# Kernel tuning notes

Measured on AMD Instinct MI355X. Metric: run time of the kernel, lower is better.

## Reference

```python
import jax, jax.numpy as jnp
import numpy as np

B, C, CI, H, W = 4, 256, 128, 64, 64  # batch, in_channels, inter_channels, spatial
EPS = 1e-5


def conv1x1(x, w, b):
    # x: [b,c,h,w], w: [o,c], b: [o] -> [b,o,h,w]
    return jnp.einsum('bchw,oc->bohw', x, w) + b[None, :, None, None]


def setup_inputs() -> dict:
    key = jax.random.key(0)
    ks = jax.random.split(key, 16)
    s_in = 1.0 / np.sqrt(C)
    s_mid = 1.0 / np.sqrt(CI)
    inp = {
        'feats_all': jax.random.normal(ks[0], (B, C, H, W), dtype=jnp.float32),
        'human_feats': jax.random.normal(ks[1], (B, C, H, W), dtype=jnp.float32),
        'g_w': jax.random.uniform(ks[2], (CI, C), jnp.float32, -s_in, s_in),
        'g_b': jax.random.uniform(ks[3], (CI,), jnp.float32, -s_in, s_in),
        'theta_w': jax.random.uniform(ks[4], (CI, C), jnp.float32, -s_in, s_in),
        'theta_b': jax.random.uniform(ks[5], (CI,), jnp.float32, -s_in, s_in),
        'phi_w': jax.random.uniform(ks[6], (CI, C), jnp.float32, -s_in, s_in),
        'phi_b': jax.random.uniform(ks[7], (CI,), jnp.float32, -s_in, s_in),
        'human_theta_w': jax.random.uniform(ks[8], (CI, C), jnp.float32, -s_in, s_in),
        'human_theta_b': jax.random.uniform(ks[9], (CI,), jnp.float32, -s_in, s_in),
        'human_phi_w': jax.random.uniform(ks[10], (CI, C), jnp.float32, -s_in, s_in),
        'human_phi_b': jax.random.uniform(ks[11], (CI,), jnp.float32, -s_in, s_in),
        'W_w': jax.random.uniform(ks[12], (C, CI), jnp.float32, -s_mid, s_mid),
        'W_b': jax.random.uniform(ks[13], (C,), jnp.float32, -s_mid, s_mid),
        'bn_gamma': jax.random.normal(ks[14], (C,), dtype=jnp.float32) * 0.1 + 1.0,
        'bn_beta': jax.random.normal(ks[15], (C,), dtype=jnp.float32) * 0.1,
        'bn_mean': jnp.zeros((C,), jnp.float32),
        'bn_var': jnp.ones((C,), jnp.float32),
    }
    return inp


def reference(feats_all, human_feats, g_w, g_b, theta_w, theta_b, phi_w, phi_b,
              human_theta_w, human_theta_b, human_phi_w, human_phi_b,
              W_w, W_b, bn_gamma, bn_beta, bn_mean, bn_var):
    b = feats_all.shape[0]
    n = H * W
    scale = CI ** -0.5

    # human attention map: softmax over keys of scaled QK^T
    hq = conv1x1(human_feats, human_theta_w, human_theta_b).reshape(b, CI, n)  # [b,ci,n]
    hk = conv1x1(human_feats, human_phi_w, human_phi_b).reshape(b, CI, n)
    human_map = jax.nn.softmax(scale * jnp.einsum('bcq,bck->bqk', hq, hk), axis=-1)

    # standard non-local map on feats_all
    th = conv1x1(feats_all, theta_w, theta_b).reshape(b, CI, n)
    ph = conv1x1(feats_all, phi_w, phi_b).reshape(b, CI, n)
    f = jax.nn.softmax(scale * jnp.einsum('bcq,bck->bqk', th, ph), axis=-1)

    g_x = conv1x1(feats_all, g_w, g_b).reshape(b, CI, n)  # [b,ci,n]

    attn = (human_map + f) * 0.5                          # [b,n,n]
    y = jnp.einsum('bqk,bck->bcq', attn, g_x)             # [b,ci,n]
    y = y.reshape(b, CI, H, W)

    wy = conv1x1(y, W_w, W_b)                             # [b,C,H,W]
    # BatchNorm2d (eval mode, running stats)
    inv = bn_gamma / jnp.sqrt(bn_var + EPS)
    out = (wy - bn_mean[None, :, None, None]) * inv[None, :, None, None] + bn_beta[None, :, None, None]
    return out
```

## Files before the change

### kernel.cpp

```cpp
#include <hip/hip_runtime.h>

#define DEVI __device__ __forceinline__

typedef float f32x4 __attribute__((ext_vector_type(4)));
typedef unsigned int u32x4 __attribute__((ext_vector_type(4)));
typedef unsigned int u32x2 __attribute__((ext_vector_type(2)));
typedef __bf16 bf16x8 __attribute__((ext_vector_type(8)));

#define NB 4
#define CIN 256
#define CI_ 128
#define NN 4096
#define SCALE 0.08838834764831845f

typedef unsigned short us;

DEVI us f2bf(float f) {
  unsigned int x = __float_as_uint(f);
  x += 0x7FFFu + ((x >> 16) & 1u);
  return (us)(x >> 16);
}

DEVI unsigned pack2(float a, float b) {
  return (unsigned)f2bf(a) | ((unsigned)f2bf(b) << 16);
}

DEVI f32x4 mfma16(u32x4 a, u32x4 b, f32x4 c) {
  return __builtin_amdgcn_mfma_f32_16x16x32_bf16(
      __builtin_bit_cast(bf16x8, a), __builtin_bit_cast(bf16x8, b), c, 0, 0, 0);
}

DEVI void gload16(const void* g, void* l) {
  __builtin_amdgcn_global_load_lds(
      (const __attribute__((address_space(1))) void*)g,
      (__attribute__((address_space(3))) void*)l, 16, 0, 0);
}

__global__ __launch_bounds__(256) void wcvt_kernel(
    const float* __restrict__ hth_w, const float* __restrict__ hph_w,
    const float* __restrict__ th_w, const float* __restrict__ ph_w,
    const float* __restrict__ g_w, const float* __restrict__ Ww,
    us* __restrict__ wb) {
  const float* srcs[6] = {hth_w, hph_w, th_w, ph_w, g_w, Ww};
  const float* s = srcs[blockIdx.y];
  us* d = wb + blockIdx.y * 32768;
  int idx = (blockIdx.x * 256 + threadIdx.x) * 4;
  f32x4 v = *(const f32x4*)(s + idx);
  u32x2 o;
  o[0] = pack2(v[0], v[1]);
  o[1] = pack2(v[2], v[3]);
  *(u32x2*)(d + idx) = o;
}

__global__ __launch_bounds__(256) void proj_kernel(
    const float* __restrict__ feats, const float* __restrict__ human,
    const float* __restrict__ g_b, const float* __restrict__ th_b,
    const float* __restrict__ ph_b, const float* __restrict__ hth_b,
    const float* __restrict__ hph_b, const us* __restrict__ wb,
    us* __restrict__ hqT, us* __restrict__ hkT,
    us* __restrict__ thT, us* __restrict__ phT, us* __restrict__ gP) {
  __shared__ alignas(16) us xf[64 * 256];
  __shared__ alignas(16) us xh[64 * 256];
  const int t = threadIdx.x;
  const int b = blockIdx.y;
  const int n0 = blockIdx.x * 64;
  const int w = t >> 6, l = t & 63, g16 = l >> 4, l15 = l & 15;

  for (int which = 0; which < 2; ++which) {
    const float* src = which ? human : feats;
    us* dst = which ? xh : xf;
    for (int i = 0; i < 16; ++i) {
      int e = (i * 256 + t) * 4;
      int c = e >> 6, nn = e & 63;
      f32x4 v = *(const f32x4*)(src + (size_t)(b * CIN + c) * NN + n0 + nn);
#pragma unroll
      for (int j = 0; j < 4; ++j) {
        int row = nn + j;
        dst[row * 256 + (c ^ ((row & 15) << 3))] = f2bf(v[j]);
      }
    }
  }
  __syncthreads();

  const float* pb[4] = {hth_b, hph_b, th_b, ph_b};
  us* pout[4] = {hqT, hkT, thT, phT};

  u32x4 afrag[8];
  const int arow = w * 16 + l15;
  for (int p = 0; p < 4; ++p) {
    const us* tile = (p < 2) ? xh : xf;
    if (p == 0 || p == 2) {
#pragma unroll
      for (int s = 0; s < 8; ++s)
        afrag[s] = *(const u32x4*)((const char*)tile + arow * 512 +
                                   (((s << 6) | (g16 << 4)) ^ (l15 << 4)));
    }
    const us* wbp = wb + p * 32768;
    for (int nt = 0; nt < 8; ++nt) {
      f32x4 acc = {0.f, 0.f, 0.f, 0.f};
#pragma unroll
      for (int s = 0; s < 8; ++s) {
        u32x4 bf = *(const u32x4*)(wbp + (nt * 16 + l15) * 256 + s * 32 + g16 * 8);
        acc = mfma16(afrag[s], bf, acc);
      }
      float bias = pb[p][nt * 16 + l15];
#pragma unroll
      for (int r = 0; r < 4; ++r) {
        int nrow = n0 + w * 16 + g16 * 4 + r;
        pout[p][((size_t)b * NN + nrow) * CI_ + nt * 16 + l15] = f2bf(acc[r] + bias);
      }
    }
  }

  const us* wbg = wb + 4 * 32768;
  u32x4 ag[2][8];
#pragma unroll
  for (int mt = 0; mt < 2; ++mt)
#pragma unroll
    for (int s = 0; s < 8; ++s)
      ag[mt][s] = *(const u32x4*)(wbg + (w * 32 + mt * 16 + l15) * 256 + s * 32 + g16 * 8);
  float gb[2][4];
#pragma unroll
  for (int mt = 0; mt < 2; ++mt)
#pragma unroll
    for (int r = 0; r < 4; ++r) gb[mt][r] = g_b[w * 32 + mt * 16 + g16 * 4 + r];
  for (int nt = 0; nt < 4; ++nt) {
    f32x4 acc0 = {0.f, 0.f, 0.f, 0.f}, acc1 = {0.f, 0.f, 0.f, 0.f};
#pragma unroll
    for (int s = 0; s < 8; ++s) {
      u32x4 bf = *(const u32x4*)((const char*)xf + (nt * 16 + l15) * 512 +
                                 ((s * 64 + g16 * 16) ^ (l15 << 4)));
      acc0 = mfma16(ag[0][s], bf, acc0);
      acc1 = mfma16(ag[1][s], bf, acc1);
    }
#pragma unroll
    for (int r = 0; r < 4; ++r) {
      int ci0 = w * 32 + g16 * 4 + r;
      gP[((size_t)b * CI_ + ci0) * NN + n0 + nt * 16 + l15] = f2bf(acc0[r] + gb[0][r]);
      gP[((size_t)b * CI_ + ci0 + 16) * NN + n0 + nt * 16 + l15] = f2bf(acc1[r] + gb[1][r]);
    }
  }
}

__global__ __launch_bounds__(128, 2) void attn_kernel(
    const us* __restrict__ hqT, const us* __restrict__ hkT,
    const us* __restrict__ thT, const us* __restrict__ phT,
    const us* __restrict__ gP, us* __restrict__ PY, float* __restrict__ PL) {
  __shared__ alignas(16) us sK[2][32 * 128];
  __shared__ alignas(16) us sV[2][64 * 64];
  __shared__ alignas(16) us sPp[2][16 * 64];
  const int t = threadIdx.x, w = t >> 6, l = t & 63, g16 = l >> 4, l15 = l & 15;
  const int id = blockIdx.x;
  const int xcd = id & 7, b = xcd & 3, path = xcd >> 2;
  const int r2 = id >> 3, h = r2 & 1, chunk = r2 >> 1;
  const int q0 = chunk * 64, kb = h * 2048;
  const us* Qsrc = path ? thT : hqT;
  const char* Kb = (const char*)(path ? phT : hkT) + (size_t)b * NN * 256;
  const char* Vb = (const char*)gP + (size_t)b * CI_ * NN * 2;

  u32x4 aQ[2][4];
#pragma unroll
  for (int qs = 0; qs < 2; ++qs)
#pragma unroll
    for (int s = 0; s < 4; ++s)
      aQ[qs][s] = *(const u32x4*)(Qsrc +
          ((size_t)b * NN + q0 + w * 32 + qs * 16 + l15) * CI_ + s * 32 + g16 * 8);

  f32x4 Y[2][8];
#pragma unroll
  for (int qs = 0; qs < 2; ++qs)
#pragma unroll
    for (int dt = 0; dt < 8; ++dt) Y[qs][dt] = {0.f, 0.f, 0.f, 0.f};
  float lsum[2] = {0.f, 0.f};

  auto stage = [&](int k0, int buf) {
#pragma unroll
    for (int i = 0; i < 4; ++i) {
      int krow = w * 16 + i * 4 + (l >> 4);
      gload16(Kb + (size_t)(k0 + krow) * 256 + (((l & 15) * 16) ^ ((krow & 7) << 4)),
              (char*)sK[buf] + (w * 16 + i * 4) * 256);
    }
#pragma unroll
    for (int i = 0; i < 4; ++i) {
      int j = w * 32 + i * 8 + (l >> 3);
      int srcin = ((l & 7) * 16) ^ ((j & 7) << 4);
      gload16(Vb + (size_t)(2 * j + (srcin >> 6)) * (NN * 2) + (size_t)k0 * 2 + (srcin & 63),
              (char*)sV[buf] + (w * 32 + i * 8) * 128);
    }
  };

  stage(kb, 0);
  __syncthreads();
  for (int kt = 0; kt < 64; ++kt) {
    const int cur = kt & 1;
    if (kt < 63) stage(kb + (kt + 1) * 32, cur ^ 1);
    const char* sKc = (const char*)sK[cur];
    const char* sVc = (const char*)sV[cur];
    float pv[2][2][4];
#pragma unroll
    for (int nt = 0; nt < 2; ++nt) {
      f32x4 a0 = {0.f, 0.f, 0.f, 0.f}, a1 = {0.f, 0.f, 0.f, 0.f};
#pragma unroll
      for (int s = 0; s < 4; ++s) {
        u32x4 bk = *(const u32x4*)(sKc + (nt * 16 + l15) * 256 +
                                   ((s * 64 + g16 * 16) ^ ((l15 & 7) << 4)));
        a0 = mfma16(bk, aQ[0][s], a0);
        a1 = mfma16(bk, aQ[1][s], a1);
      }
#pragma unroll
      for (int r = 0; r < 4; ++r) {
        float p0 = __expf(a0[r] * SCALE), p1 = __expf(a1[r] * SCALE);
        lsum[0] += p0;
        lsum[1] += p1;
        pv[0][nt][r] = p0;
        pv[1][nt][r] = p1;
      }
    }
#pragma unroll
    for (int qs = 0; qs < 2; ++qs)
#pragma unroll
      for (int nt = 0; nt < 2; ++nt) {
        u32x2 pw;
        pw[0] = pack2(pv[qs][nt][0], pv[qs][nt][1]);
        pw[1] = pack2(pv[qs][nt][2], pv[qs][nt][3]);
        *(u32x2*)((char*)sPp[w] + (qs * 8 + (l15 >> 1)) * 128 +
                  (((l15 & 1) * 64 + nt * 32 + g16 * 8) ^ ((l15 >> 1) << 4))) = pw;
      }
    u32x4 aP[2];
#pragma unroll
    for (int qs = 0; qs < 2; ++qs)
      aP[qs] = *(const u32x4*)((char*)sPp[w] + (qs * 8 + (l15 >> 1)) * 128 +
                               (((l15 & 1) * 64 + g16 * 16) ^ ((l15 >> 1) << 4)));
#pragma unroll
    for (int dt = 0; dt < 8; ++dt) {
      int dd = dt * 16 + l15;
      u32x4 bv = *(const u32x4*)(sVc + (dd >> 1) * 128 +
                                 (((dd & 1) * 64 + g16 * 16) ^ (((dd >> 1) & 7) << 4)));
      Y[0][dt] = mfma16(aP[0], bv, Y[0][dt]);
      Y[1][dt] = mfma16(aP[1], bv, Y[1][dt]);
    }
    __syncthreads();
  }

  const int bp = b * 2 + path;
#pragma unroll
  for (int qs = 0; qs < 2; ++qs) {
    float v = lsum[qs];
    v += __shfl_xor(v, 16);
    v += __shfl_xor(v, 32);
    if (g16 == 0)
      PL[(size_t)(h * 8 + bp) * NN + q0 + w * 32 + qs * 16 + l15] = v;
#pragma unroll
    for (int dt = 0; dt < 8; ++dt)
#pragma unroll
      for (int r = 0; r < 4; ++r)
        PY[(size_t)(h * 8 + bp) * (NN * CI_) +
           (size_t)(q0 + w * 32 + qs * 16 + g16 * 4 + r) * CI_ + dt * 16 + l15] =
            f2bf(Y[qs][dt][r]);
  }
}

__global__ __launch_bounds__(256) void wout_kernel(
    const us* __restrict__ PY, const float* __restrict__ PL,
    const us* __restrict__ wb, const float* __restrict__ Wb,
    const float* __restrict__ gamma, const float* __restrict__ beta,
    const float* __restrict__ mean, const float* __restrict__ var,
    float* __restrict__ out) {
  __shared__ alignas(16) us sY[64 * 128];
  const int t = threadIdx.x, w = t >> 6, l = t & 63, g16 = l >> 4, l15 = l & 15;
  const int n0 = blockIdx.x * 64;
  const int ob = blockIdx.y * 64;
  const int b = blockIdx.z;

  {
    const int row = t >> 2, cg = t & 3;
    const int n = n0 + row;
    float ls[2];
#pragma unroll
    for (int p = 0; p < 2; ++p) {
      int bpi = b * 2 + p;
      ls[p] = 0.5f / (PL[(size_t)bpi * NN + n] + PL[(size_t)(8 + bpi) * NN + n]);
    }
    float acc[32];
#pragma unroll
    for (int e = 0; e < 32; ++e) acc[e] = 0.f;
#pragma unroll
    for (int p = 0; p < 2; ++p) {
      float sc = ls[p];
#pragma unroll
      for (int hh = 0; hh < 2; ++hh) {
        const us* src = PY + (size_t)(hh * 8 + b * 2 + p) * (NN * CI_) +
                        (size_t)n * CI_ + cg * 32;
#pragma unroll
        for (int j = 0; j < 4; ++j) {
          u32x4 v = *(const u32x4*)(src + j * 8);
#pragma unroll
          for (int e = 0; e < 4; ++e) {
            unsigned u = v[e];
            acc[j * 8 + 2 * e] += __uint_as_float(u << 16) * sc;
            acc[j * 8 + 2 * e + 1] += __uint_as_float(u & 0xFFFF0000u) * sc;
          }
        }
      }
    }
#pragma unroll
    for (int j = 0; j < 4; ++j) {
      u32x4 o;
#pragma unroll
      for (int e = 0; e < 4; ++e)
        o[e] = pack2(acc[j * 8 + 2 * e], acc[j * 8 + 2 * e + 1]);
      *(u32x4*)((char*)sY + row * 256 + ((cg * 64 + j * 16) ^ ((row & 7) << 4))) = o;
    }
  }

  const us* wbw = wb + 5 * 32768;
  u32x4 aW[4];
  const int orow = ob + w * 16 + l15;
#pragma unroll
  for (int s = 0; s < 4; ++s)
    aW[s] = *(const u32x4*)(wbw + orow * 128 + s * 32 + g16 * 8);
  float wbias[4], inv_[4], mu[4], bt[4];
#pragma unroll
  for (int r = 0; r < 4; ++r) {
    int o = ob + w * 16 + g16 * 4 + r;
    wbias[r] = Wb[o];
    inv_[r] = gamma[o] * rsqrtf(var[o] + 1e-5f);
    mu[r] = mean[o];
    bt[r] = beta[o];
  }
  __syncthreads();

  for (int nt = 0; nt < 4; ++nt) {
    f32x4 acc = {0.f, 0.f, 0.f, 0.f};
#pragma unroll
    for (int s = 0; s < 4; ++s) {
      u32x4 bf = *(const u32x4*)((const char*)sY + (nt * 16 + l15) * 256 +
                                 (((s << 6) | (g16 << 4)) ^ ((l15 & 7) << 4)));
      acc = mfma16(aW[s], bf, acc);
    }
#pragma unroll
    for (int r = 0; r < 4; ++r) {
      int o = ob + w * 16 + g16 * 4 + r;
      out[((size_t)b * CIN + o) * NN + n0 + nt * 16 + l15] =
          (acc[r] + wbias[r] - mu[r]) * inv_[r] + bt[r];
    }
  }
}

extern "C" void kernel_launch(void* const* d_in, const int* in_sizes, int n_in,
                              void* d_out, int out_size, void* d_ws, size_t ws_size,
                              hipStream_t stream) {
  const float* feats = (const float*)d_in[0];
  const float* human = (const float*)d_in[1];
  const float* g_w = (const float*)d_in[2];
  const float* g_b = (const float*)d_in[3];
  const float* th_w = (const float*)d_in[4];
  const float* th_b = (const float*)d_in[5];
  const float* ph_w = (const float*)d_in[6];
  const float* ph_b = (const float*)d_in[7];
  const float* hth_w = (const float*)d_in[8];
  const float* hth_b = (const float*)d_in[9];
  const float* hph_w = (const float*)d_in[10];
  const float* hph_b = (const float*)d_in[11];
  const float* Ww = (const float*)d_in[12];
  const float* Wb = (const float*)d_in[13];
  const float* gamma = (const float*)d_in[14];
  const float* beta = (const float*)d_in[15];
  const float* mean = (const float*)d_in[16];
  const float* var = (const float*)d_in[17];

  us* ws = (us*)d_ws;
  const size_t SZ = (size_t)NB * NN * CI_;
  us* hqT = ws;
  us* hkT = ws + SZ;
  us* thT = ws + 2 * SZ;
  us* phT = ws + 3 * SZ;
  us* gP = ws + 4 * SZ;
  us* PY = ws + 5 * SZ;
  float* PL = (float*)(ws + 5 * SZ + 8388608);
  us* wb = ws + 5 * SZ + 8388608 + 131072;

  wcvt_kernel<<<dim3(32, 6), 256, 0, stream>>>(hth_w, hph_w, th_w, ph_w, g_w, Ww, wb);
  proj_kernel<<<dim3(64, 4), 256, 0, stream>>>(feats, human, g_b, th_b, ph_b,
                                               hth_b, hph_b, wb, hqT, hkT, thT,
                                               phT, gP);
  attn_kernel<<<1024, 128, 0, stream>>>(hqT, hkT, thT, phT, gP, PY, PL);
  wout_kernel<<<dim3(64, 4, 4), 256, 0, stream>>>(PY, PL, wb, Wb, gamma, beta,
                                                  mean, var, (float*)d_out);
}
```

Before: 157.2 us.

## Restructure attention kernel with larger key tiles, in-block key split, exp2 prescale

The attention kernel now uses 256-thread blocks that each own 64 queries across all keys. The four waves split each 128-key tile, and their partial outputs are reduced through shared memory instead of being written as two half-range partials to global memory. The softmax scale times log2(e) is folded into the Q projection so the kernel can call a raw exp2. Float-to-bf16 packing uses the hardware v_cvt_pk_bf16_f32 instruction, and the projection input staging loads two channels per thread to pack pairs. This cuts global partial traffic and raises MFMA reuse per loaded K/V tile, at the cost of more registers, a single-buffered stage with extra barriers, and a shared-memory reduction epilogue.

```diff
diff --git a/kernel.cpp b/kernel.cpp
--- a/kernel.cpp
+++ b/kernel.cpp
@@ -11,7 +11,7 @@
 #define CIN 256
 #define CI_ 128
 #define NN 4096
-#define SCALE 0.08838834764831845f
+#define QSCALE 0.12752792233895158f
 
 typedef unsigned short us;
 
@@ -21,8 +21,18 @@
   return (us)(x >> 16);
 }
 
-DEVI unsigned pack2(float a, float b) {
-  return (unsigned)f2bf(a) | ((unsigned)f2bf(b) << 16);
+DEVI unsigned cvtpk(float lo, float hi) {
+  unsigned r;
+  asm("v_cvt_pk_bf16_f32 %0, %1, %2" : "=v"(r) : "v"(lo), "v"(hi));
+  return r;
+}
+
+DEVI float exp2fast(float x) {
+#if __has_builtin(__builtin_amdgcn_exp2f)
+  return __builtin_amdgcn_exp2f(x);
+#else
+  return exp2f(x);
+#endif
 }
 
 DEVI f32x4 mfma16(u32x4 a, u32x4 b, f32x4 c) {
@@ -47,8 +57,8 @@
   int idx = (blockIdx.x * 256 + threadIdx.x) * 4;
   f32x4 v = *(const f32x4*)(s + idx);
   u32x2 o;
-  o[0] = pack2(v[0], v[1]);
-  o[1] = pack2(v[2], v[3]);
+  o[0] = cvtpk(v[0], v[1]);
+  o[1] = cvtpk(v[2], v[3]);
   *(u32x2*)(d + idx) = o;
 }
 
@@ -65,18 +75,22 @@
   const int b = blockIdx.y;
   const int n0 = blockIdx.x * 64;
   const int w = t >> 6, l = t & 63, g16 = l >> 4, l15 = l & 15;
+  const int tg = t >> 4, tl = t & 15;
 
   for (int which = 0; which < 2; ++which) {
     const float* src = which ? human : feats;
     us* dst = which ? xh : xf;
-    for (int i = 0; i < 16; ++i) {
-      int e = (i * 256 + t) * 4;
-      int c = e >> 6, nn = e & 63;
-      f32x4 v = *(const f32x4*)(src + (size_t)(b * CIN + c) * NN + n0 + nn);
+#pragma unroll
+    for (int i = 0; i < 8; ++i) {
+      int p = i * 16 + tg;
+      const float* s0 = src + (size_t)(b * CIN + 2 * p) * NN + n0 + tl * 4;
+      f32x4 v0 = *(const f32x4*)s0;
+      f32x4 v1 = *(const f32x4*)(s0 + NN);
 #pragma unroll
       for (int j = 0; j < 4; ++j) {
-        int row = nn + j;
-        dst[row * 256 + (c ^ ((row & 15) << 3))] = f2bf(v[j]);
+        int row = tl * 4 + j;
+        *(unsigned*)((char*)dst + row * 512 + ((4 * p) ^ ((row & 15) << 4))) =
+            cvtpk(v0[j], v1[j]);
       }
     }
   }
@@ -96,6 +110,7 @@
                                    (((s << 6) | (g16 << 4)) ^ (l15 << 4)));
     }
     const us* wbp = wb + p * 32768;
+    const float scl = (p == 0 || p == 2) ? QSCALE : 1.0f;
     for (int nt = 0; nt < 8; ++nt) {
       f32x4 acc = {0.f, 0.f, 0.f, 0.f};
 #pragma unroll
@@ -107,7 +122,8 @@
 #pragma unroll
       for (int r = 0; r < 4; ++r) {
         int nrow = n0 + w * 16 + g16 * 4 + r;
-        pout[p][((size_t)b * NN + nrow) * CI_ + nt * 16 + l15] = f2bf(acc[r] + bias);
+        pout[p][((size_t)b * NN + nrow) * CI_ + nt * 16 + l15] =
+            f2bf((acc[r] + bias) * scl);
       }
     }
   }
@@ -142,121 +158,185 @@
   }
 }
 
-__global__ __launch_bounds__(128, 2) void attn_kernel(
+__global__ __launch_bounds__(256, 2) void attn_kernel(
     const us* __restrict__ hqT, const us* __restrict__ hkT,
     const us* __restrict__ thT, const us* __restrict__ phT,
     const us* __restrict__ gP, us* __restrict__ PY, float* __restrict__ PL) {
-  __shared__ alignas(16) us sK[2][32 * 128];
-  __shared__ alignas(16) us sV[2][64 * 64];
-  __shared__ alignas(16) us sPp[2][16 * 64];
+  __shared__ alignas(16) us sK[128 * 128];
+  __shared__ alignas(16) us sV[128 * 128];
+  __shared__ alignas(16) us sP[64 * 128];
+
   const int t = threadIdx.x, w = t >> 6, l = t & 63, g16 = l >> 4, l15 = l & 15;
   const int id = blockIdx.x;
-  const int xcd = id & 7, b = xcd & 3, path = xcd >> 2;
-  const int r2 = id >> 3, h = r2 & 1, chunk = r2 >> 1;
-  const int q0 = chunk * 64, kb = h * 2048;
-  const us* Qsrc = path ? thT : hqT;
-  const char* Kb = (const char*)(path ? phT : hkT) + (size_t)b * NN * 256;
-  const char* Vb = (const char*)gP + (size_t)b * CI_ * NN * 2;
-
-  u32x4 aQ[2][4];
-#pragma unroll
-  for (int qs = 0; qs < 2; ++qs)
+  const int bp = id & 7, b = bp & 3, path = bp >> 2;
+  const int q0 = (id >> 3) * 64;
+  const us* Qs = (path ? thT : hqT) + (size_t)b * NN * CI_;
+  const char* Kb = (const char*)((path ? phT : hkT) + (size_t)b * NN * CI_);
+  const char* Vb = (const char*)(gP + (size_t)b * CI_ * NN);
+
+  u32x4 aQ[4][4];
+#pragma unroll
+  for (int qs = 0; qs < 4; ++qs)
 #pragma unroll
     for (int s = 0; s < 4; ++s)
-      aQ[qs][s] = *(const u32x4*)(Qsrc +
-          ((size_t)b * NN + q0 + w * 32 + qs * 16 + l15) * CI_ + s * 32 + g16 * 8);
-
-  f32x4 Y[2][8];
-#pragma unroll
-  for (int qs = 0; qs < 2; ++qs)
+      aQ[qs][s] = *(const u32x4*)(Qs + (size_t)(q0 + qs * 16 + l15) * CI_ +
+                                  s * 32 + g16 * 8);
+
+  f32x4 Y[4][8];
+#pragma unroll
+  for (int qs = 0; qs < 4; ++qs)
 #pragma unroll
     for (int dt = 0; dt < 8; ++dt) Y[qs][dt] = {0.f, 0.f, 0.f, 0.f};
-  float lsum[2] = {0.f, 0.f};
-
-  auto stage = [&](int k0, int buf) {
-#pragma unroll
-    for (int i = 0; i < 4; ++i) {
-      int krow = w * 16 + i * 4 + (l >> 4);
-      gload16(Kb + (size_t)(k0 + krow) * 256 + (((l & 15) * 16) ^ ((krow & 7) << 4)),
-              (char*)sK[buf] + (w * 16 + i * 4) * 256);
-    }
-#pragma unroll
-    for (int i = 0; i < 4; ++i) {
-      int j = w * 32 + i * 8 + (l >> 3);
-      int srcin = ((l & 7) * 16) ^ ((j & 7) << 4);
-      gload16(Vb + (size_t)(2 * j + (srcin >> 6)) * (NN * 2) + (size_t)k0 * 2 + (srcin & 63),
-              (char*)sV[buf] + (w * 32 + i * 8) * 128);
+  float lsum[4] = {0.f, 0.f, 0.f, 0.f};
+
+  const int rr = w * 32 + (l >> 4);
+  const int uK = l & 15;
+
+  auto stage = [&](int k0) {
+#pragma unroll
+    for (int i = 0; i < 8; ++i) {
+      int row = rr + i * 4;
+      int su = (uK ^ (row & 7)) << 4;
+      gload16(Kb + (((size_t)(k0 + row)) << 8) + su,
+              (char*)sK + ((w * 8 + i) << 10));
+      gload16(Vb + ((size_t)row << 13) + ((size_t)k0 << 1) + su,
+              (char*)sV + ((w * 8 + i) << 10));
     }
   };
 
-  stage(kb, 0);
-  __syncthreads();
-  for (int kt = 0; kt < 64; ++kt) {
-    const int cur = kt & 1;
-    if (kt < 63) stage(kb + (kt + 1) * 32, cur ^ 1);
-    const char* sKc = (const char*)sK[cur];
-    const char* sVc = (const char*)sV[cur];
-    float pv[2][2][4];
-#pragma unroll
-    for (int nt = 0; nt < 2; ++nt) {
-      f32x4 a0 = {0.f, 0.f, 0.f, 0.f}, a1 = {0.f, 0.f, 0.f, 0.f};
-#pragma unroll
-      for (int s = 0; s < 4; ++s) {
-        u32x4 bk = *(const u32x4*)(sKc + (nt * 16 + l15) * 256 +
-                                   ((s * 64 + g16 * 16) ^ ((l15 & 7) << 4)));
-        a0 = mfma16(bk, aQ[0][s], a0);
-        a1 = mfma16(bk, aQ[1][s], a1);
-      }
-#pragma unroll
-      for (int r = 0; r < 4; ++r) {
-        float p0 = __expf(a0[r] * SCALE), p1 = __expf(a1[r] * SCALE);
-        lsum[0] += p0;
-        lsum[1] += p1;
-        pv[0][nt][r] = p0;
-        pv[1][nt][r] = p1;
-      }
-    }
-#pragma unroll
-    for (int qs = 0; qs < 2; ++qs)
-#pragma unroll
-      for (int nt = 0; nt < 2; ++nt) {
+  stage(0);
+  __syncthreads();
+
+  for (int kt = 0; kt < 32; ++kt) {
+#pragma unroll
+    for (int kk = 0; kk < 2; ++kk) {
+      const int krow = 32 * w + kk * 16 + l15;
+      u32x4 ak[4];
+#pragma unroll
+      for (int s = 0; s < 4; ++s)
+        ak[s] = *(const u32x4*)((const char*)sK + krow * 256 +
+                                ((s * 64 + g16 * 16) ^ ((l15 & 7) << 4)));
+      f32x4 acc[4];
+#pragma unroll
+      for (int qs = 0; qs < 4; ++qs) acc[qs] = {0.f, 0.f, 0.f, 0.f};
+      __builtin_amdgcn_s_setprio(1);
+#pragma unroll
+      for (int s = 0; s < 4; ++s)
+#pragma unroll
+        for (int qs = 0; qs < 4; ++qs)
+          acc[qs] = mfma16(ak[s], aQ[qs][s], acc[qs]);
+      __builtin_amdgcn_s_setprio(0);
+#pragma unroll
+      for (int qs = 0; qs < 4; ++qs) {
+#pragma unroll
+        for (int r = 0; r < 4; ++r) {
+          float p = exp2fast(acc[qs][r]);
+          lsum[qs] += p;
+          acc[qs][r] = p;
+        }
         u32x2 pw;
-        pw[0] = pack2(pv[qs][nt][0], pv[qs][nt][1]);
-        pw[1] = pack2(pv[qs][nt][2], pv[qs][nt][3]);
-        *(u32x2*)((char*)sPp[w] + (qs * 8 + (l15 >> 1)) * 128 +
-                  (((l15 & 1) * 64 + nt * 32 + g16 * 8) ^ ((l15 >> 1) << 4))) = pw;
-      }
-    u32x4 aP[2];
-#pragma unroll
-    for (int qs = 0; qs < 2; ++qs)
-      aP[qs] = *(const u32x4*)((char*)sPp[w] + (qs * 8 + (l15 >> 1)) * 128 +
-                               (((l15 & 1) * 64 + g16 * 16) ^ ((l15 >> 1) << 4)));
+        pw[0] = cvtpk(acc[qs][0], acc[qs][1]);
+        pw[1] = cvtpk(acc[qs][2], acc[qs][3]);
+        int q = qs * 16 + l15;
+        *(u32x2*)((char*)sP + q * 256 +
+                  ((64 * w + kk * 32 + g16 * 8) ^ ((l15 & 7) << 4))) = pw;
+      }
+    }
+    u32x4 aP[4];
+#pragma unroll
+    for (int qs = 0; qs < 4; ++qs) {
+      int q = qs * 16 + l15;
+      aP[qs] = *(const u32x4*)((const char*)sP + q * 256 +
+                               ((64 * w + g16 * 16) ^ ((l15 & 7) << 4)));
+    }
+    __builtin_amdgcn_s_setprio(1);
 #pragma unroll
     for (int dt = 0; dt < 8; ++dt) {
-      int dd = dt * 16 + l15;
-      u32x4 bv = *(const u32x4*)(sVc + (dd >> 1) * 128 +
-                                 (((dd & 1) * 64 + g16 * 16) ^ (((dd >> 1) & 7) << 4)));
-      Y[0][dt] = mfma16(aP[0], bv, Y[0][dt]);
-      Y[1][dt] = mfma16(aP[1], bv, Y[1][dt]);
-    }
+      int vrow = dt * 16 + l15;
+      u32x4 bv = *(const u32x4*)((const char*)sV + vrow * 256 +
+                                 ((64 * w + g16 * 16) ^ ((l15 & 7) << 4)));
+#pragma unroll
+      for (int qs = 0; qs < 4; ++qs) Y[qs][dt] = mfma16(aP[qs], bv, Y[qs][dt]);
+    }
+    __builtin_amdgcn_s_setprio(0);
     __syncthreads();
-  }
-
-  const int bp = b * 2 + path;
-#pragma unroll
-  for (int qs = 0; qs < 2; ++qs) {
+    if (kt < 31) {
+      stage((kt + 1) * 128);
+      __syncthreads();
+    }
+  }
+
+  float* psum = (float*)sP;
+#pragma unroll
+  for (int qs = 0; qs < 4; ++qs) {
     float v = lsum[qs];
     v += __shfl_xor(v, 16);
     v += __shfl_xor(v, 32);
-    if (g16 == 0)
-      PL[(size_t)(h * 8 + bp) * NN + q0 + w * 32 + qs * 16 + l15] = v;
-#pragma unroll
-    for (int dt = 0; dt < 8; ++dt)
-#pragma unroll
-      for (int r = 0; r < 4; ++r)
-        PY[(size_t)(h * 8 + bp) * (NN * CI_) +
-           (size_t)(q0 + w * 32 + qs * 16 + g16 * 4 + r) * CI_ + dt * 16 + l15] =
-            f2bf(Y[qs][dt][r]);
+    lsum[qs] = v;
+  }
+  if (g16 == 0) {
+#pragma unroll
+    for (int qs = 0; qs < 4; ++qs) psum[w * 64 + qs * 16 + l15] = lsum[qs];
+  }
+
+  float* regA = (float*)sK;
+  float* regB = (float*)sV;
+  auto ywrite = [&](float* reg) {
+#pragma unroll
+    for (int qs = 0; qs < 4; ++qs)
+#pragma unroll
+      for (int dt = 0; dt < 8; ++dt) {
+        int d = dt * 16 + l15;
+        *(f32x4*)((char*)reg + d * 256 +
+                  ((qs * 64 + g16 * 16) ^ ((l15 & 7) << 4))) = Y[qs][dt];
+      }
+  };
+  auto yadd = [&](const float* reg) {
+#pragma unroll
+    for (int qs = 0; qs < 4; ++qs)
+#pragma unroll
+      for (int dt = 0; dt < 8; ++dt) {
+        int d = dt * 16 + l15;
+        f32x4 v = *(const f32x4*)((const char*)reg + d * 256 +
+                                  ((qs * 64 + g16 * 16) ^ ((l15 & 7) << 4)));
+        Y[qs][dt] += v;
+      }
+  };
+
+  if (w >= 2) ywrite(w == 2 ? regA : regB);
+  __syncthreads();
+  if (w == 0) yadd(regA);
+  if (w == 1) {
+    yadd(regB);
+    ywrite(regB);
+  }
+  if (w == 3) {
+    float s = psum[l] + psum[64 + l] + psum[128 + l] + psum[192 + l];
+    PL[(size_t)bp * NN + q0 + l] = s;
+  }
+  __syncthreads();
+  if (w == 0) {
+    yadd(regB);
+    ywrite(regA);
+  }
+  __syncthreads();
+  {
+    const int q = l;
+#pragma unroll
+    for (int o = 0; o < 4; ++o) {
+      float vals[8];
+#pragma unroll
+      for (int j = 0; j < 8; ++j) {
+        int d = w * 32 + o * 8 + j;
+        vals[j] = *(const float*)((const char*)regA + d * 256 +
+                                  ((q * 4) ^ ((d & 7) << 4)));
+      }
+      u32x4 pk;
+#pragma unroll
+      for (int e = 0; e < 4; ++e) pk[e] = cvtpk(vals[2 * e], vals[2 * e + 1]);
+      *(u32x4*)((char*)PY + (size_t)bp * (NN * CI_ * 2) +
+                (size_t)(q0 + q) * 256 + w * 64 + o * 16) = pk;
+    }
   }
 }
 
@@ -275,31 +355,22 @@
   {
     const int row = t >> 2, cg = t & 3;
     const int n = n0 + row;
-    float ls[2];
+    float acc[32];
+#pragma unroll
+    for (int e = 0; e < 32; ++e) acc[e] = 0.f;
 #pragma unroll
     for (int p = 0; p < 2; ++p) {
-      int bpi = b * 2 + p;
-      ls[p] = 0.5f / (PL[(size_t)bpi * NN + n] + PL[(size_t)(8 + bpi) * NN + n]);
-    }
-    float acc[32];
-#pragma unroll
-    for (int e = 0; e < 32; ++e) acc[e] = 0.f;
-#pragma unroll
-    for (int p = 0; p < 2; ++p) {
-      float sc = ls[p];
-#pragma unroll
-      for (int hh = 0; hh < 2; ++hh) {
-        const us* src = PY + (size_t)(hh * 8 + b * 2 + p) * (NN * CI_) +
-                        (size_t)n * CI_ + cg * 32;
-#pragma unroll
-        for (int j = 0; j < 4; ++j) {
-          u32x4 v = *(const u32x4*)(src + j * 8);
-#pragma unroll
-          for (int e = 0; e < 4; ++e) {
-            unsigned u = v[e];
-            acc[j * 8 + 2 * e] += __uint_as_float(u << 16) * sc;
-            acc[j * 8 + 2 * e + 1] += __uint_as_float(u & 0xFFFF0000u) * sc;
-          }
+      int bpi = p * 4 + b;
+      float sc = 0.5f / PL[(size_t)bpi * NN + n];
+      const us* src = PY + (size_t)bpi * (NN * CI_) + (size_t)n * CI_ + cg * 32;
+#pragma unroll
+      for (int j = 0; j < 4; ++j) {
+        u32x4 v = *(const u32x4*)(src + j * 8);
+#pragma unroll
+        for (int e = 0; e < 4; ++e) {
+          unsigned u = v[e];
+          acc[j * 8 + 2 * e] += __uint_as_float(u << 16) * sc;
+          acc[j * 8 + 2 * e + 1] += __uint_as_float(u & 0xFFFF0000u) * sc;
         }
       }
     }
@@ -308,7 +379,7 @@
       u32x4 o;
 #pragma unroll
       for (int e = 0; e < 4; ++e)
-        o[e] = pack2(acc[j * 8 + 2 * e], acc[j * 8 + 2 * e + 1]);
+        o[e] = cvtpk(acc[j * 8 + 2 * e], acc[j * 8 + 2 * e + 1]);
       *(u32x4*)((char*)sY + row * 256 + ((cg * 64 + j * 16) ^ ((row & 7) << 4))) = o;
     }
   }
@@ -377,14 +448,14 @@
   us* phT = ws + 3 * SZ;
   us* gP = ws + 4 * SZ;
   us* PY = ws + 5 * SZ;
-  float* PL = (float*)(ws + 5 * SZ + 8388608);
-  us* wb = ws + 5 * SZ + 8388608 + 131072;
+  float* PL = (float*)(ws + 5 * SZ + 4194304);
+  us* wb = ws + 5 * SZ + 4194304 + 65536;
 
   wcvt_kernel<<<dim3(32, 6), 256, 0, stream>>>(hth_w, hph_w, th_w, ph_w, g_w, Ww, wb);
   proj_kernel<<<dim3(64, 4), 256, 0, stream>>>(feats, human, g_b, th_b, ph_b,
                                                hth_b, hph_b, wb, hqT, hkT, thT,
                                                phT, gP);
-  attn_kernel<<<1024, 128, 0, stream>>>(hqT, hkT, thT, phT, gP, PY, PL);
+  attn_kernel<<<512, 256, 0, stream>>>(hqT, hkT, thT, phT, gP, PY, PL);
   wout_kernel<<<dim3(64, 4, 4), 256, 0, stream>>>(PY, PL, wb, Wb, gamma, beta,
                                                   mean, var, (float*)d_out);
 }
```

Measured after the change: 255.8 us. 1.63x slower.
